# Kernel optimization log

Measured on AMD Instinct MI355X. Metric: run time of the kernel, lower is better.

The kernel has to match this reference:

```python
import jax, jax.numpy as jnp
import numpy as np

B, Q, T, H, M, K, V = 4, 1024, 1024, 16, 1024, 64, 64


def _masked_softmax(logits, active, axis):
    # jnp softmax(..., where=active, initial=0.0): max taken over active entries
    # with initial value 0.0; inactive positions get probability 0.
    neg = jnp.where(active, logits, -jnp.inf)
    m = jnp.maximum(jnp.max(neg, axis=axis, keepdims=True), 0.0)
    e = jnp.where(active, jnp.exp(neg - m), 0.0)
    return e / jnp.sum(e, axis=axis, keepdims=True)


def _entropy_bits(p, where, axis):
    # entropy in bits over `axis`, counting only `where` entries; 0*log0 -> 0
    mask = (where > 0) & (p > 0)
    pl = jnp.where(mask, p * jnp.log2(jnp.where(mask, p, 1.0)), 0.0)
    return -jnp.sum(pl, axis=axis)


def setup_inputs() -> dict:
    key = jax.random.key(0)
    k1, k2, k3, k4, k5, k6 = jax.random.split(key, 6)
    mscale = 1.0 / np.sqrt(M)
    vscale = 1.0 / np.sqrt(V)
    qinput = jax.random.normal(k1, (B, Q, M), jnp.float32)
    kvinput = jax.random.normal(k2, (B, T, M), jnp.float32)
    qmask = jnp.zeros((B, Q), jnp.float32)
    tmask = jnp.zeros((B, T), jnp.float32)
    # causal combined mask: 1 = ignore future target positions
    qtmask = jnp.broadcast_to(jnp.triu(jnp.ones((Q, T), jnp.float32), k=1), (B, Q, T))
    wq = jax.random.normal(k3, (H, M, K), jnp.float32) * mscale
    wk = jax.random.normal(k4, (H, M, K), jnp.float32) * mscale
    wv = jax.random.normal(k5, (H, M, V), jnp.float32) * mscale
    wo = jax.random.normal(k6, (H, V, M), jnp.float32) * vscale
    return {"qinput": qinput, "kvinput": kvinput, "qmask": qmask, "tmask": tmask,
            "qtmask": qtmask, "wq": wq, "wk": wk, "wv": wv, "wo": wo}


def reference(qinput, kvinput, qmask, tmask, qtmask, wq, wk, wv, wo):
    kscale = 1.0 / np.sqrt(K)
    qm = qmask[:, :, None]                      # bq1
    tm = tmask[:, None, :]                      # b1t
    logits_mask = jnp.maximum(tm, qtmask)       # bqt, 1 = ignore

    query = jnp.einsum('hmd,bqm->bhqd', wq, qinput)
    key_ = jnp.einsum('hmd,btm->bhtd', wk, kvinput)
    val = jnp.einsum('hmd,btm->bhtd', wv, kvinput)

    alogit = jnp.einsum('bhqd,bhtd->bhqt', query, key_)
    active = (1.0 - logits_mask)[:, None, :, :] > 0          # bhqt (broadcast)
    att = _masked_softmax(alogit * kscale, active, axis=3)   # bhqt

    # attention entropy statistics
    occu = 1.0 - logits_mask                                  # bqt
    row_occu = jnp.sum(occu, axis=2, keepdims=True)[:, None, :, :]  # b1q1
    active_cols = jnp.max(occu, axis=1)                       # bt
    target_marg = jnp.sum(att * row_occu, axis=(1, 2))        # bt
    target_sum = jnp.sum(target_marg, axis=1, keepdims=True)
    target_norm = target_marg / target_sum
    target_entr = _entropy_bits(target_norm, active_cols, axis=1)  # b
    c = jnp.sum(active_cols, axis=1)
    scaled_entr = target_entr / jnp.log2(c)

    pre = jnp.einsum('bhqt,bhtd->bhqd', att, val)
    out = jnp.einsum('hdm,bhqd->bqm', wo, pre)
    out = out * (1.0 - qm)
    return (out, scaled_entr)
```

## Files before the change

kernel.cpp:

```cpp
#include <hip/hip_runtime.h>
#include <hip/hip_bf16.h>

typedef unsigned short u16;
typedef __attribute__((ext_vector_type(8))) short bf16x8;
typedef __attribute__((ext_vector_type(4))) float f32x4;

#define MFMA(a, b, c) __builtin_amdgcn_mfma_f32_16x16x32_bf16(a, b, c, 0, 0, 0)

__device__ inline u16 f2bf(float f) {
    union { __hip_bfloat16 b; u16 u; } cv;
    cv.b = __float2bfloat16(f);
    return cv.u;
}

__device__ inline f32x4 zero4() {
    f32x4 v; v[0] = 0.f; v[1] = 0.f; v[2] = 0.f; v[3] = 0.f; return v;
}

__device__ inline void gl_lds16(const u16* g, u16* l) {
    __builtin_amdgcn_global_load_lds(
        (const __attribute__((address_space(1))) u16*)(g),
        (__attribute__((address_space(3))) u16*)(l), 16, 0, 0);
}

__global__ __launch_bounds__(256) void cvt2_kernel(const float* __restrict__ qa, const float* __restrict__ kva,
                                                   u16* __restrict__ oq, u16* __restrict__ okv) {
    int bid = blockIdx.x;
    const float* in = (bid < 4096) ? qa : kva;
    u16* out = (bid < 4096) ? oq : okv;
    int i = (((bid & 4095) * 256) + threadIdx.x) * 4;
    float4 v = *(const float4*)(in + i);
    u16 o[4] = { f2bf(v.x), f2bf(v.y), f2bf(v.z), f2bf(v.w) };
    *(uint2*)(out + i) = *(const uint2*)o;
}

__global__ __launch_bounds__(256) void wtrans4_kernel(const float* __restrict__ wq, const float* __restrict__ wk,
                                                      const float* __restrict__ wv, const float* __restrict__ wo,
                                                      u16* __restrict__ W3, u16* __restrict__ Wot) {
    __shared__ float tile[64][65];
    int by = blockIdx.y, h = blockIdx.z, tid = threadIdx.x;
    const float* src; u16* dst; int R, C, ho, r0, c0;
    if (by == 3) { src = wo; dst = Wot; R = 64; C = 1024; ho = 64; r0 = 0; c0 = blockIdx.x * 64; }
    else {
        src = (by == 0) ? wq : (by == 1) ? wk : wv;
        dst = W3 + (size_t)by * 1024 * 1024;
        R = 1024; C = 64; ho = 64 * 1024; r0 = blockIdx.x * 64; c0 = 0;
    }
    const float* s = src + (size_t)h * R * C;
#pragma unroll
    for (int k = 0; k < 16; k++) {
        int idx = tid + k * 256;
        int i = idx >> 6, j = idx & 63;
        tile[i][j] = s[(size_t)(r0 + i) * C + (c0 + j)];
    }
    __syncthreads();
    u16* d = dst + (size_t)h * ho;
#pragma unroll
    for (int k = 0; k < 16; k++) {
        int idx = tid + k * 256;
        int j = idx >> 6, i = idx & 63;
        d[(size_t)(c0 + j) * 1024 + (r0 + i)] = f2bf(tile[i][j]);
    }
}

__global__ __launch_bounds__(256) void proj_kernel(const u16* __restrict__ Xq, const u16* __restrict__ Xkv,
                                                   const u16* __restrict__ W3,
                                                   u16* __restrict__ Qp, u16* __restrict__ Kp,
                                                   u16* __restrict__ Vt) {
    __shared__ __align__(16) u16 As[128 * 32];
    __shared__ __align__(16) u16 Bs[128 * 32];
    int tid = threadIdx.x;
    int ny = blockIdx.y;
    int sel = ny >> 3;
    const u16* A  = (sel == 0) ? Xq : Xkv;
    const u16* Bt = W3 + (size_t)sel * 1024 * 1024;
    int m0 = blockIdx.x * 128, n0 = (ny & 7) * 128;
    int w = tid >> 6, lane = tid & 63, quad = lane >> 4, c = lane & 15;
    int mw = (w & 1) * 64, nw = (w >> 1) * 64;
    f32x4 acc[4][4];
#pragma unroll
    for (int i = 0; i < 4; i++)
#pragma unroll
        for (int j = 0; j < 4; j++) acc[i][j] = zero4();

    for (int k0 = 0; k0 < 1024; k0 += 32) {
        __syncthreads();
#pragma unroll
        for (int s = 0; s < 2; s++) {
            int ch = s * 256 + w * 64 + lane;
            int r = ch >> 2, cc = (ch & 3) * 8;
            gl_lds16(&A[(size_t)(m0 + r) * 1024 + k0 + cc],  &As[(s * 256 + w * 64) * 8]);
            gl_lds16(&Bt[(size_t)(n0 + r) * 1024 + k0 + cc], &Bs[(s * 256 + w * 64) * 8]);
        }
        asm volatile("s_waitcnt vmcnt(0)" ::: "memory");
        __syncthreads();
        bf16x8 af[4], bfr[4];
#pragma unroll
        for (int i = 0; i < 4; i++) af[i] = *(const bf16x8*)&As[(mw + i * 16 + c) * 32 + quad * 8];
#pragma unroll
        for (int j = 0; j < 4; j++) bfr[j] = *(const bf16x8*)&Bs[(nw + j * 16 + c) * 32 + quad * 8];
#pragma unroll
        for (int i = 0; i < 4; i++)
#pragma unroll
            for (int j = 0; j < 4; j++) acc[i][j] = MFMA(af[i], bfr[j], acc[i][j]);
    }
#pragma unroll
    for (int i = 0; i < 4; i++) {
#pragma unroll
        for (int r = 0; r < 4; r++) {
            int row = m0 + mw + i * 16 + quad * 4 + r;
#pragma unroll
            for (int j = 0; j < 4; j++) {
                int col = n0 + nw + j * 16 + c;
                u16 v = f2bf(acc[i][j][r]);
                if (sel == 0)      Qp[(size_t)row * 1024 + col] = v;
                else if (sel == 1) Kp[(size_t)row * 1024 + col] = v;
                else {
                    int b = row >> 10, t = row & 1023;
                    Vt[((size_t)(b * 16 + (col >> 6)) * 64 + (col & 63)) * 1024 + t] = v;
                }
            }
        }
    }
}

__global__ __launch_bounds__(256) void gemmo_kernel(const u16* __restrict__ A, const u16* __restrict__ Bt,
                                                    float* __restrict__ Cf, const float* __restrict__ qmask) {
    __shared__ __align__(16) u16 As[128 * 32];
    __shared__ __align__(16) u16 Bs[128 * 32];
    int tid = threadIdx.x;
    int m0 = blockIdx.x * 128, n0 = blockIdx.y * 128;
    int w = tid >> 6, lane = tid & 63, quad = lane >> 4, c = lane & 15;
    int mw = (w & 1) * 64, nw = (w >> 1) * 64;
    f32x4 acc[4][4];
#pragma unroll
    for (int i = 0; i < 4; i++)
#pragma unroll
        for (int j = 0; j < 4; j++) acc[i][j] = zero4();

    for (int k0 = 0; k0 < 1024; k0 += 32) {
        __syncthreads();
#pragma unroll
        for (int s = 0; s < 2; s++) {
            int ch = s * 256 + w * 64 + lane;
            int r = ch >> 2, cc = (ch & 3) * 8;
            gl_lds16(&A[(size_t)(m0 + r) * 1024 + k0 + cc],  &As[(s * 256 + w * 64) * 8]);
            gl_lds16(&Bt[(size_t)(n0 + r) * 1024 + k0 + cc], &Bs[(s * 256 + w * 64) * 8]);
        }
        asm volatile("s_waitcnt vmcnt(0)" ::: "memory");
        __syncthreads();
        bf16x8 af[4], bfr[4];
#pragma unroll
        for (int i = 0; i < 4; i++) af[i] = *(const bf16x8*)&As[(mw + i * 16 + c) * 32 + quad * 8];
#pragma unroll
        for (int j = 0; j < 4; j++) bfr[j] = *(const bf16x8*)&Bs[(nw + j * 16 + c) * 32 + quad * 8];
#pragma unroll
        for (int i = 0; i < 4; i++)
#pragma unroll
            for (int j = 0; j < 4; j++) acc[i][j] = MFMA(af[i], bfr[j], acc[i][j]);
    }
#pragma unroll
    for (int i = 0; i < 4; i++) {
#pragma unroll
        for (int r = 0; r < 4; r++) {
            int row = m0 + mw + i * 16 + quad * 4 + r;
            float scale = 1.0f - qmask[row];
#pragma unroll
            for (int j = 0; j < 4; j++) {
                int col = n0 + nw + j * 16 + c;
                Cf[(size_t)row * 1024 + col] = acc[i][j][r] * scale;
            }
        }
    }
}

__global__ __launch_bounds__(256) void attn_kernel(const u16* __restrict__ Qp, const u16* __restrict__ Kp,
                                                   const u16* __restrict__ Vt, u16* __restrict__ Pre,
                                                   float* __restrict__ marg) {
    __shared__ __align__(16) u16 Ks[64 * 64];
    __shared__ __align__(16) u16 Vs[64 * 64];
    __shared__ __align__(16) u16 plds[4][16 * 72];
    __shared__ float colbuf[1024];
    int tid = threadIdx.x;
    int bx = blockIdx.x, h = blockIdx.y, b = blockIdx.z;
    int w = tid >> 6, lane = tid & 63, quad = lane >> 4, c = lane & 15;
    int tmax = 64 * (bx + 1);
    for (int i = tid; i < tmax; i += 256) colbuf[i] = 0.f;

    int q0 = bx * 64 + w * 16;
    const u16* qrow = Qp + (size_t)(b * 1024 + q0 + c) * 1024 + h * 64;
    bf16x8 aq0 = *(const bf16x8*)(qrow + quad * 8);
    bf16x8 aq1 = *(const bf16x8*)(qrow + 32 + quad * 8);

    const u16* kb = Kp + (size_t)b * 1024 * 1024 + h * 64;
    const u16* vb = Vt + (size_t)(b * 16 + h) * 64 * 1024;
    u16* pl = plds[w];
    const float sc = 0.125f * 1.4426950408889634f;

    int idx0 = w * 64 + lane;
    int row0 = idx0 >> 3;
    int lu = (idx0 & 7) ^ (row0 & 7);
    int sw = c & 7;
    int su0 = (quad ^ sw) * 8;
    int su1 = ((quad ^ 4) ^ sw) * 8;

    f32x4 o[4];
#pragma unroll
    for (int i = 0; i < 4; i++) o[i] = zero4();
    float l[4] = {0.f, 0.f, 0.f, 0.f};
    int qg[4];
#pragma unroll
    for (int r = 0; r < 4; r++) qg[r] = q0 + quad * 4 + r;
    int tlast = 64 * bx;

    for (int t0 = 0; t0 <= tlast; t0 += 64) {
        __syncthreads();
        gl_lds16(kb + (size_t)(t0 + row0) * 1024 + lu * 8,      Ks + w * 64 * 8);
        gl_lds16(kb + (size_t)(t0 + row0 + 32) * 1024 + lu * 8, Ks + (256 + w * 64) * 8);
        gl_lds16(vb + (size_t)row0 * 1024 + t0 + lu * 8,        Vs + w * 64 * 8);
        gl_lds16(vb + (size_t)(row0 + 32) * 1024 + t0 + lu * 8, Vs + (256 + w * 64) * 8);
        asm volatile("s_waitcnt vmcnt(0)" ::: "memory");
        __syncthreads();
        f32x4 s[4];
#pragma unroll
        for (int j = 0; j < 4; j++) {
            const u16* kr = Ks + (j * 16 + c) * 64;
            bf16x8 b0 = *(const bf16x8*)(kr + su0);
            bf16x8 b1 = *(const bf16x8*)(kr + su1);
            s[j] = MFMA(aq0, b0, zero4());
            s[j] = MFMA(aq1, b1, s[j]);
        }
        if (t0 < tlast) {
#pragma unroll
            for (int j = 0; j < 4; j++)
#pragma unroll
                for (int r = 0; r < 4; r++) {
                    float e = exp2f(s[j][r] * sc);
                    l[r] += e;
                    pl[(quad * 4 + r) * 72 + j * 16 + c] = f2bf(e);
                }
        } else {
#pragma unroll
            for (int j = 0; j < 4; j++) {
                int t = t0 + j * 16 + c;
#pragma unroll
                for (int r = 0; r < 4; r++) {
                    float e = (t <= qg[r]) ? exp2f(s[j][r] * sc) : 0.f;
                    l[r] += e;
                    pl[(quad * 4 + r) * 72 + j * 16 + c] = f2bf(e);
                }
            }
        }
        asm volatile("s_waitcnt lgkmcnt(0)" ::: "memory");
        bf16x8 ap0 = *(const bf16x8*)&pl[c * 72 + quad * 8];
        bf16x8 ap1 = *(const bf16x8*)&pl[c * 72 + 32 + quad * 8];
#pragma unroll
        for (int vt = 0; vt < 4; vt++) {
            const u16* vr = Vs + (vt * 16 + c) * 64;
            bf16x8 bv0 = *(const bf16x8*)(vr + su0);
            bf16x8 bv1 = *(const bf16x8*)(vr + su1);
            o[vt] = MFMA(ap0, bv0, o[vt]);
            o[vt] = MFMA(ap1, bv1, o[vt]);
        }
    }

    float invl[4];
#pragma unroll
    for (int r = 0; r < 4; r++) {
        float lr = l[r];
#pragma unroll
        for (int d = 1; d < 16; d <<= 1) lr += __shfl_xor(lr, d);
        invl[r] = 1.0f / lr;
    }
#pragma unroll
    for (int vt = 0; vt < 4; vt++)
#pragma unroll
        for (int r = 0; r < 4; r++) {
            size_t row = (size_t)(b * 1024 + q0 + quad * 4 + r);
            Pre[row * 1024 + h * 64 + vt * 16 + c] = f2bf(o[vt][r] * invl[r]);
        }

    float wr[4];
#pragma unroll
    for (int r = 0; r < 4; r++) wr[r] = (float)(qg[r] + 1) * invl[r];
    for (int t0 = 0; t0 <= tlast; t0 += 64) {
        __syncthreads();
        gl_lds16(kb + (size_t)(t0 + row0) * 1024 + lu * 8,      Ks + w * 64 * 8);
        gl_lds16(kb + (size_t)(t0 + row0 + 32) * 1024 + lu * 8, Ks + (256 + w * 64) * 8);
        asm volatile("s_waitcnt vmcnt(0)" ::: "memory");
        __syncthreads();
        f32x4 s[4];
#pragma unroll
        for (int j = 0; j < 4; j++) {
            const u16* kr = Ks + (j * 16 + c) * 64;
            bf16x8 b0 = *(const bf16x8*)(kr + su0);
            bf16x8 b1 = *(const bf16x8*)(kr + su1);
            s[j] = MFMA(aq0, b0, zero4());
            s[j] = MFMA(aq1, b1, s[j]);
        }
        float a[4];
        if (t0 < tlast) {
#pragma unroll
            for (int j = 0; j < 4; j++) {
                float aj = 0.f;
#pragma unroll
                for (int r = 0; r < 4; r++) aj += exp2f(s[j][r] * sc) * wr[r];
                aj += __shfl_xor(aj, 16);
                aj += __shfl_xor(aj, 32);
                a[j] = aj;
            }
        } else {
#pragma unroll
            for (int j = 0; j < 4; j++) {
                int t = t0 + j * 16 + c;
                float aj = 0.f;
#pragma unroll
                for (int r = 0; r < 4; r++) aj += (t <= qg[r]) ? exp2f(s[j][r] * sc) * wr[r] : 0.f;
                aj += __shfl_xor(aj, 16);
                aj += __shfl_xor(aj, 32);
                a[j] = aj;
            }
        }
        float v = (quad == 0) ? a[0] : (quad == 1) ? a[1] : (quad == 2) ? a[2] : a[3];
        atomicAdd(&colbuf[t0 + lane], v);
    }
    __syncthreads();
    for (int t = tid; t < tmax; t += 256) atomicAdd(&marg[b * 1024 + t], colbuf[t]);
}

__global__ __launch_bounds__(256) void entropy_kernel(const float* __restrict__ marg, float* __restrict__ out) {
    int b = blockIdx.x, tid = threadIdx.x;
    __shared__ float red[256];
    float s = 0.f;
    for (int t = tid; t < 1024; t += 256) s += marg[b * 1024 + t];
    red[tid] = s; __syncthreads();
    for (int k = 128; k > 0; k >>= 1) { if (tid < k) red[tid] += red[tid + k]; __syncthreads(); }
    float tot = red[0];
    __syncthreads();
    float e = 0.f;
    for (int t = tid; t < 1024; t += 256) {
        float p = marg[b * 1024 + t] / tot;
        if (p > 0.f) e -= p * log2f(p);
    }
    red[tid] = e; __syncthreads();
    for (int k = 128; k > 0; k >>= 1) { if (tid < k) red[tid] += red[tid + k]; __syncthreads(); }
    if (tid == 0) out[b] = red[0] * 0.1f;
}

extern "C" void kernel_launch(void* const* d_in, const int* in_sizes, int n_in,
                              void* d_out, int out_size, void* d_ws, size_t ws_size,
                              hipStream_t stream) {
    const float* qinput  = (const float*)d_in[0];
    const float* kvinput = (const float*)d_in[1];
    const float* qmask   = (const float*)d_in[2];
    const float* wq = (const float*)d_in[5];
    const float* wk = (const float*)d_in[6];
    const float* wv = (const float*)d_in[7];
    const float* wo = (const float*)d_in[8];

    char* ws = (char*)d_ws;
    const size_t MB = 1024 * 1024;
    u16* Xq   = (u16*)(ws + 0);
    u16* Xkv  = (u16*)(ws + 8 * MB);
    u16* W3   = (u16*)(ws + 16 * MB);
    u16* Wot  = (u16*)(ws + 22 * MB);
    u16* Qp   = (u16*)(ws + 24 * MB);
    u16* Kp   = (u16*)(ws + 32 * MB);
    u16* Vt   = (u16*)(ws + 40 * MB);
    float* marg = (float*)(ws + 48 * MB);
    u16* Pre = Xq;
    float* out = (float*)d_out;

    cvt2_kernel<<<8192, 256, 0, stream>>>(qinput, kvinput, Xq, Xkv);
    wtrans4_kernel<<<dim3(16, 4, 16), 256, 0, stream>>>(wq, wk, wv, wo, W3, Wot);
    proj_kernel<<<dim3(32, 24), 256, 0, stream>>>(Xq, Xkv, W3, Qp, Kp, Vt);

    hipMemsetAsync(marg, 0, 4096 * sizeof(float), stream);
    attn_kernel<<<dim3(16, 16, 4), 256, 0, stream>>>(Qp, Kp, Vt, Pre, marg);
    entropy_kernel<<<4, 256, 0, stream>>>(marg, out + (size_t)4 * 1024 * 1024);
    gemmo_kernel<<<dim3(32, 8), 256, 0, stream>>>(Pre, Wot, out, qmask);
}
```

Before: 261.9 us.

## Pair causal query tiles per block, double-buffer K/V, transpose V via LDS

The attention kernel now runs 512 threads per block and gives each block two query tiles, bx and 15-bx, so causal work is balanced across blocks. The grid is halved to match. K and V tiles are double-buffered, and the next tile is prefetched with partial vmcnt waits so loads overlap MFMA work. Separately, the projection kernel stages the V output in LDS and writes Vt as coalesced 16-byte vectors instead of strided scalar stores. The costs are more LDS, a larger block that may limit occupancy, and idle waves in blocks where the short tile finishes early.

```diff
diff --git a/kernel.cpp b/kernel.cpp
--- a/kernel.cpp
+++ b/kernel.cpp
@@ -21,6 +21,10 @@
     __builtin_amdgcn_global_load_lds(
         (const __attribute__((address_space(1))) u16*)(g),
         (__attribute__((address_space(3))) u16*)(l), 16, 0, 0);
+}
+
+__device__ inline void barrier_nodrain() {
+    asm volatile("s_waitcnt lgkmcnt(0)\ns_barrier" ::: "memory");
 }
 
 __global__ __launch_bounds__(256) void cvt2_kernel(const float* __restrict__ qa, const float* __restrict__ kva,
@@ -69,6 +73,7 @@
                                                    u16* __restrict__ Vt) {
     __shared__ __align__(16) u16 As[128 * 32];
     __shared__ __align__(16) u16 Bs[128 * 32];
+    __shared__ __align__(16) u16 Ts[128 * 136];
     int tid = threadIdx.x;
     int ny = blockIdx.y;
     int sel = ny >> 3;
@@ -104,22 +109,36 @@
 #pragma unroll
             for (int j = 0; j < 4; j++) acc[i][j] = MFMA(af[i], bfr[j], acc[i][j]);
     }
-#pragma unroll
-    for (int i = 0; i < 4; i++) {
-#pragma unroll
-        for (int r = 0; r < 4; r++) {
-            int row = m0 + mw + i * 16 + quad * 4 + r;
-#pragma unroll
-            for (int j = 0; j < 4; j++) {
-                int col = n0 + nw + j * 16 + c;
-                u16 v = f2bf(acc[i][j][r]);
-                if (sel == 0)      Qp[(size_t)row * 1024 + col] = v;
-                else if (sel == 1) Kp[(size_t)row * 1024 + col] = v;
-                else {
-                    int b = row >> 10, t = row & 1023;
-                    Vt[((size_t)(b * 16 + (col >> 6)) * 64 + (col & 63)) * 1024 + t] = v;
-                }
-            }
+    if (sel < 2) {
+        u16* C_ = (sel == 0) ? Qp : Kp;
+#pragma unroll
+        for (int i = 0; i < 4; i++)
+#pragma unroll
+            for (int r = 0; r < 4; r++) {
+                int row = m0 + mw + i * 16 + quad * 4 + r;
+#pragma unroll
+                for (int j = 0; j < 4; j++)
+                    C_[(size_t)row * 1024 + n0 + nw + j * 16 + c] = f2bf(acc[i][j][r]);
+            }
+    } else {
+#pragma unroll
+        for (int i = 0; i < 4; i++)
+#pragma unroll
+            for (int r = 0; r < 4; r++) {
+                int rowL = mw + i * 16 + quad * 4 + r;
+#pragma unroll
+                for (int j = 0; j < 4; j++)
+                    Ts[(nw + j * 16 + c) * 136 + rowL] = f2bf(acc[i][j][r]);
+            }
+        __syncthreads();
+        int bb = m0 >> 10, tbase = m0 & 1023;
+#pragma unroll
+        for (int it = 0; it < 8; it++) {
+            int linear = tid + it * 256;
+            int colL = linear >> 4, r0 = (linear & 15) * 8;
+            int colG = n0 + colL;
+            bf16x8 v = *(const bf16x8*)&Ts[colL * 136 + r0];
+            *(bf16x8*)&Vt[(((size_t)(bb * 16 + (colG >> 6)) * 64) + (colG & 63)) * 1024 + tbase + r0] = v;
         }
     }
 }
@@ -174,20 +193,23 @@
     }
 }
 
-__global__ __launch_bounds__(256) void attn_kernel(const u16* __restrict__ Qp, const u16* __restrict__ Kp,
+__global__ __launch_bounds__(512) void attn_kernel(const u16* __restrict__ Qp, const u16* __restrict__ Kp,
                                                    const u16* __restrict__ Vt, u16* __restrict__ Pre,
                                                    float* __restrict__ marg) {
-    __shared__ __align__(16) u16 Ks[64 * 64];
-    __shared__ __align__(16) u16 Vs[64 * 64];
-    __shared__ __align__(16) u16 plds[4][16 * 72];
+    __shared__ __align__(16) u16 Ks[2][64 * 64];
+    __shared__ __align__(16) u16 Vs[2][64 * 64];
+    __shared__ __align__(16) u16 plds[8][16 * 72];
     __shared__ float colbuf[1024];
     int tid = threadIdx.x;
     int bx = blockIdx.x, h = blockIdx.y, b = blockIdx.z;
     int w = tid >> 6, lane = tid & 63, quad = lane >> 4, c = lane & 15;
-    int tmax = 64 * (bx + 1);
-    for (int i = tid; i < tmax; i += 256) colbuf[i] = 0.f;
-
-    int q0 = bx * 64 + w * 16;
+    int nA = 16 - bx, nB = bx + 1;
+    int tmaxb = nA * 64;
+    for (int i = tid; i < tmaxb; i += 512) colbuf[i] = 0.f;
+
+    int nq = (w < 4) ? nA : nB;
+    int q0 = (w < 4) ? ((15 - bx) * 64 + w * 16) : (bx * 64 + (w - 4) * 16);
+
     const u16* qrow = Qp + (size_t)(b * 1024 + q0 + c) * 1024 + h * 64;
     bf16x8 aq0 = *(const bf16x8*)(qrow + quad * 8);
     bf16x8 aq1 = *(const bf16x8*)(qrow + 32 + quad * 8);
@@ -197,12 +219,13 @@
     u16* pl = plds[w];
     const float sc = 0.125f * 1.4426950408889634f;
 
-    int idx0 = w * 64 + lane;
-    int row0 = idx0 >> 3;
-    int lu = (idx0 & 7) ^ (row0 & 7);
+    int rowS = tid >> 3;
+    int lu = (tid & 7) ^ (rowS & 7);
     int sw = c & 7;
     int su0 = (quad ^ sw) * 8;
     int su1 = ((quad ^ 4) ^ sw) * 8;
+    u16* ldsK = &Ks[0][0] + w * 512;
+    u16* ldsV = &Vs[0][0] + w * 512;
 
     f32x4 o[4];
 #pragma unroll
@@ -211,56 +234,64 @@
     int qg[4];
 #pragma unroll
     for (int r = 0; r < 4; r++) qg[r] = q0 + quad * 4 + r;
-    int tlast = 64 * bx;
-
-    for (int t0 = 0; t0 <= tlast; t0 += 64) {
-        __syncthreads();
-        gl_lds16(kb + (size_t)(t0 + row0) * 1024 + lu * 8,      Ks + w * 64 * 8);
-        gl_lds16(kb + (size_t)(t0 + row0 + 32) * 1024 + lu * 8, Ks + (256 + w * 64) * 8);
-        gl_lds16(vb + (size_t)row0 * 1024 + t0 + lu * 8,        Vs + w * 64 * 8);
-        gl_lds16(vb + (size_t)(row0 + 32) * 1024 + t0 + lu * 8, Vs + (256 + w * 64) * 8);
-        asm volatile("s_waitcnt vmcnt(0)" ::: "memory");
-        __syncthreads();
-        f32x4 s[4];
-#pragma unroll
-        for (int j = 0; j < 4; j++) {
-            const u16* kr = Ks + (j * 16 + c) * 64;
-            bf16x8 b0 = *(const bf16x8*)(kr + su0);
-            bf16x8 b1 = *(const bf16x8*)(kr + su1);
-            s[j] = MFMA(aq0, b0, zero4());
-            s[j] = MFMA(aq1, b1, s[j]);
-        }
-        if (t0 < tlast) {
-#pragma unroll
-            for (int j = 0; j < 4; j++)
-#pragma unroll
-                for (int r = 0; r < 4; r++) {
-                    float e = exp2f(s[j][r] * sc);
-                    l[r] += e;
-                    pl[(quad * 4 + r) * 72 + j * 16 + c] = f2bf(e);
+
+    gl_lds16(kb + (size_t)rowS * 1024 + lu * 8, ldsK);
+    gl_lds16(vb + (size_t)rowS * 1024 + lu * 8, ldsV);
+    for (int ci = 0; ci < nA; ci++) {
+        int bf = ci & 1;
+        barrier_nodrain();
+        if (ci + 1 < nA) {
+            gl_lds16(kb + (size_t)((ci + 1) * 64 + rowS) * 1024 + lu * 8, ldsK + (bf ^ 1) * 4096);
+            gl_lds16(vb + (size_t)rowS * 1024 + (ci + 1) * 64 + lu * 8,  ldsV + (bf ^ 1) * 4096);
+            asm volatile("s_waitcnt vmcnt(2)" ::: "memory");
+        } else {
+            asm volatile("s_waitcnt vmcnt(0)" ::: "memory");
+        }
+        asm volatile("s_barrier" ::: "memory");
+        if (ci < nq) {
+            const u16* Kb = &Ks[bf][0];
+            const u16* Vb = &Vs[bf][0];
+            f32x4 s[4];
+#pragma unroll
+            for (int j = 0; j < 4; j++) {
+                const u16* kr = Kb + (j * 16 + c) * 64;
+                bf16x8 b0 = *(const bf16x8*)(kr + su0);
+                bf16x8 b1 = *(const bf16x8*)(kr + su1);
+                s[j] = MFMA(aq0, b0, zero4());
+                s[j] = MFMA(aq1, b1, s[j]);
+            }
+            if (ci < nq - 1) {
+#pragma unroll
+                for (int j = 0; j < 4; j++)
+#pragma unroll
+                    for (int r = 0; r < 4; r++) {
+                        float e = exp2f(s[j][r] * sc);
+                        l[r] += e;
+                        pl[(quad * 4 + r) * 72 + j * 16 + c] = f2bf(e);
+                    }
+            } else {
+#pragma unroll
+                for (int j = 0; j < 4; j++) {
+                    int t = ci * 64 + j * 16 + c;
+#pragma unroll
+                    for (int r = 0; r < 4; r++) {
+                        float e = (t <= qg[r]) ? exp2f(s[j][r] * sc) : 0.f;
+                        l[r] += e;
+                        pl[(quad * 4 + r) * 72 + j * 16 + c] = f2bf(e);
+                    }
                 }
-        } else {
-#pragma unroll
-            for (int j = 0; j < 4; j++) {
-                int t = t0 + j * 16 + c;
-#pragma unroll
-                for (int r = 0; r < 4; r++) {
-                    float e = (t <= qg[r]) ? exp2f(s[j][r] * sc) : 0.f;
-                    l[r] += e;
-                    pl[(quad * 4 + r) * 72 + j * 16 + c] = f2bf(e);
-                }
-            }
-        }
-        asm volatile("s_waitcnt lgkmcnt(0)" ::: "memory");
-        bf16x8 ap0 = *(const bf16x8*)&pl[c * 72 + quad * 8];
-        bf16x8 ap1 = *(const bf16x8*)&pl[c * 72 + 32 + quad * 8];
-#pragma unroll
-        for (int vt = 0; vt < 4; vt++) {
-            const u16* vr = Vs + (vt * 16 + c) * 64;
-            bf16x8 bv0 = *(const bf16x8*)(vr + su0);
-            bf16x8 bv1 = *(const bf16x8*)(vr + su1);
-            o[vt] = MFMA(ap0, bv0, o[vt]);
-            o[vt] = MFMA(ap1, bv1, o[vt]);
+            }
+            asm volatile("s_waitcnt lgkmcnt(0)" ::: "memory");
+            bf16x8 ap0 = *(const bf16x8*)&pl[c * 72 + quad * 8];
+            bf16x8 ap1 = *(const bf16x8*)&pl[c * 72 + 32 + quad * 8];
+#pragma unroll
+            for (int vt = 0; vt < 4; vt++) {
+                const u16* vr = Vb + (vt * 16 + c) * 64;
+                bf16x8 bv0 = *(const bf16x8*)(vr + su0);
+                bf16x8 bv1 = *(const bf16x8*)(vr + su1);
+                o[vt] = MFMA(ap0, bv0, o[vt]);
+                o[vt] = MFMA(ap1, bv1, o[vt]);
+            }
         }
     }
 
@@ -283,49 +314,59 @@
     float wr[4];
 #pragma unroll
     for (int r = 0; r < 4; r++) wr[r] = (float)(qg[r] + 1) * invl[r];
-    for (int t0 = 0; t0 <= tlast; t0 += 64) {
-        __syncthreads();
-        gl_lds16(kb + (size_t)(t0 + row0) * 1024 + lu * 8,      Ks + w * 64 * 8);
-        gl_lds16(kb + (size_t)(t0 + row0 + 32) * 1024 + lu * 8, Ks + (256 + w * 64) * 8);
-        asm volatile("s_waitcnt vmcnt(0)" ::: "memory");
-        __syncthreads();
-        f32x4 s[4];
-#pragma unroll
-        for (int j = 0; j < 4; j++) {
-            const u16* kr = Ks + (j * 16 + c) * 64;
-            bf16x8 b0 = *(const bf16x8*)(kr + su0);
-            bf16x8 b1 = *(const bf16x8*)(kr + su1);
-            s[j] = MFMA(aq0, b0, zero4());
-            s[j] = MFMA(aq1, b1, s[j]);
-        }
-        float a[4];
-        if (t0 < tlast) {
+    asm volatile("s_waitcnt vmcnt(0)" ::: "memory");
+    __syncthreads();
+    gl_lds16(kb + (size_t)rowS * 1024 + lu * 8, ldsK);
+    for (int ci = 0; ci < nA; ci++) {
+        int bf = ci & 1;
+        barrier_nodrain();
+        if (ci + 1 < nA) {
+            gl_lds16(kb + (size_t)((ci + 1) * 64 + rowS) * 1024 + lu * 8, ldsK + (bf ^ 1) * 4096);
+            asm volatile("s_waitcnt vmcnt(1)" ::: "memory");
+        } else {
+            asm volatile("s_waitcnt vmcnt(0)" ::: "memory");
+        }
+        asm volatile("s_barrier" ::: "memory");
+        if (ci < nq) {
+            const u16* Kb = &Ks[bf][0];
+            f32x4 s[4];
 #pragma unroll
             for (int j = 0; j < 4; j++) {
-                float aj = 0.f;
-#pragma unroll
-                for (int r = 0; r < 4; r++) aj += exp2f(s[j][r] * sc) * wr[r];
-                aj += __shfl_xor(aj, 16);
-                aj += __shfl_xor(aj, 32);
-                a[j] = aj;
-            }
-        } else {
-#pragma unroll
-            for (int j = 0; j < 4; j++) {
-                int t = t0 + j * 16 + c;
-                float aj = 0.f;
-#pragma unroll
-                for (int r = 0; r < 4; r++) aj += (t <= qg[r]) ? exp2f(s[j][r] * sc) * wr[r] : 0.f;
-                aj += __shfl_xor(aj, 16);
-                aj += __shfl_xor(aj, 32);
-                a[j] = aj;
-            }
-        }
-        float v = (quad == 0) ? a[0] : (quad == 1) ? a[1] : (quad == 2) ? a[2] : a[3];
-        atomicAdd(&colbuf[t0 + lane], v);
+                const u16* kr = Kb + (j * 16 + c) * 64;
+                bf16x8 b0 = *(const bf16x8*)(kr + su0);
+                bf16x8 b1 = *(const bf16x8*)(kr + su1);
+                s[j] = MFMA(aq0, b0, zero4());
+                s[j] = MFMA(aq1, b1, s[j]);
+            }
+            float a[4];
+            if (ci < nq - 1) {
+#pragma unroll
+                for (int j = 0; j < 4; j++) {
+                    float aj = 0.f;
+#pragma unroll
+                    for (int r = 0; r < 4; r++) aj += exp2f(s[j][r] * sc) * wr[r];
+                    aj += __shfl_xor(aj, 16);
+                    aj += __shfl_xor(aj, 32);
+                    a[j] = aj;
+                }
+            } else {
+#pragma unroll
+                for (int j = 0; j < 4; j++) {
+                    int t = ci * 64 + j * 16 + c;
+                    float aj = 0.f;
+#pragma unroll
+                    for (int r = 0; r < 4; r++) aj += (t <= qg[r]) ? exp2f(s[j][r] * sc) * wr[r] : 0.f;
+                    aj += __shfl_xor(aj, 16);
+                    aj += __shfl_xor(aj, 32);
+                    a[j] = aj;
+                }
+            }
+            float v = (quad == 0) ? a[0] : (quad == 1) ? a[1] : (quad == 2) ? a[2] : a[3];
+            atomicAdd(&colbuf[ci * 64 + lane], v);
+        }
     }
     __syncthreads();
-    for (int t = tid; t < tmax; t += 256) atomicAdd(&marg[b * 1024 + t], colbuf[t]);
+    for (int t = tid; t < tmaxb; t += 512) atomicAdd(&marg[b * 1024 + t], colbuf[t]);
 }
 
 __global__ __launch_bounds__(256) void entropy_kernel(const float* __restrict__ marg, float* __restrict__ out) {
@@ -376,7 +417,7 @@
     proj_kernel<<<dim3(32, 24), 256, 0, stream>>>(Xq, Xkv, W3, Qp, Kp, Vt);
 
     hipMemsetAsync(marg, 0, 4096 * sizeof(float), stream);
-    attn_kernel<<<dim3(16, 16, 4), 256, 0, stream>>>(Qp, Kp, Vt, Pre, marg);
+    attn_kernel<<<dim3(8, 16, 4), 512, 0, stream>>>(Qp, Kp, Vt, Pre, marg);
     entropy_kernel<<<4, 256, 0, stream>>>(marg, out + (size_t)4 * 1024 * 1024);
     gemmo_kernel<<<dim3(32, 8), 256, 0, stream>>>(Pre, Wot, out, qmask);
 }
```

Result: faster. 225.2 us (-14.0%).
